# Optimization experiments

Measured on AMD Instinct MI355X. Metric: run time of the kernel, lower is better.

Reference implementation:

```python
import jax, jax.numpy as jnp
import numpy as np

# Module hyperparameters (init_kwargs)
RADIUS = 0.3
NSAMPLE = 64
NORMALIZE_XYZ = True

B, N, M, C = 8, 20000, 1024, 128  # batch, points, centers, feature channels


def setup_inputs() -> dict:
    key = jax.random.key(0)
    k1, k2, k3, k4, k5 = jax.random.split(key, 5)
    # points uniform in a side-2 cube -> each radius-0.3 ball holds ~280 pts
    xyz = jax.random.uniform(k1, (B, N, 3), jnp.float32) * 2.0
    new_xyz = jax.random.uniform(k2, (B, M, 3), jnp.float32) * 2.0
    batch_distances = jax.random.uniform(k3, (B, M), jnp.float32)
    inds = jax.random.randint(k4, (B, M), 0, N, jnp.int64)
    features = jax.random.normal(k5, (B, C, N), jnp.float32)
    return {"xyz": xyz, "new_xyz": new_xyz, "batch_distances": batch_distances,
            "inds": inds, "features": features}


def ball_query(xyz, new_xyz):
    """Standard pointnet2 ball query: first NSAMPLE indices with d^2 < r^2,
    remaining slots filled with the first in-range index. -> (B, M, NSAMPLE) int32."""
    n = xyz.shape[1]
    # (B, M, N) squared distances
    d2 = jnp.sum((new_xyz[:, :, None, :] - xyz[:, None, :, :]) ** 2, axis=-1)
    mask = d2 < (RADIUS * RADIUS)
    ar = jnp.arange(n, dtype=jnp.int32)
    # sort key: valid indices keep their index (in order), invalid pushed to back
    sort_key = jnp.where(mask, ar, ar + n)
    order = jnp.argsort(sort_key, axis=-1)[..., :NSAMPLE].astype(jnp.int32)
    cnt = jnp.sum(mask, axis=-1)  # (B, M) number of in-range points
    slot = jnp.arange(NSAMPLE, dtype=cnt.dtype)
    # slots beyond cnt are filled with the first valid index (0 if cnt == 0)
    idx = jnp.where(slot[None, None, :] < jnp.maximum(cnt, 1)[..., None],
                    order, order[..., :1])
    return idx


def reference(xyz, new_xyz, batch_distances, inds, features):
    # batch_distances / inds only accelerate the original cpp kernel; the math
    # is the plain radius search below.
    idx = ball_query(xyz, new_xyz)  # (B, M, S)
    # group xyz: (B, M, S, 3) -> (B, 3, M, S)
    grouped_xyz = jax.vmap(lambda pts, i: pts[i])(xyz, idx)
    grouped_xyz = jnp.transpose(grouped_xyz, (0, 3, 1, 2))
    grouped_xyz = grouped_xyz - jnp.transpose(new_xyz, (0, 2, 1))[..., None]
    if NORMALIZE_XYZ:
        grouped_xyz = grouped_xyz / RADIUS
    # group features: (B, C, M, S)
    grouped_features = jax.vmap(lambda f, i: f[:, i])(features, idx)
    new_features = jnp.concatenate([grouped_xyz, grouped_features], axis=1)
    return (new_features, idx)
```

## Files before the change

kernel.cpp:

```cpp
#include <hip/hip_runtime.h>

#define B_ 8
#define N_ 20000
#define M_ 1024
#define C_ 128
#define S_ 64
#define NCH_ 131
#define GD_ 7
#define NC_ (GD_*GD_*GD_)
#define SCALE_ 3.2f
#define NW_ 626
#define NWP_ 640

typedef float  vf4 __attribute__((ext_vector_type(4)));

__device__ __forceinline__ int cell_of(float x, float y, float z) {
    const int ix = (int)(x * SCALE_);
    const int iy = (int)(y * SCALE_);
    const int iz = (int)(z * SCALE_);
    return (ix * GD_ + iy) * GD_ + iz;
}

__global__ __launch_bounds__(1024) void build_grid(
    const float* __restrict__ xyz,
    float4* __restrict__ pts4,
    int* __restrict__ cst)
{
    const int b   = blockIdx.x;
    const int tid = threadIdx.x;
    __shared__ int hcnt[NC_];
    __shared__ int hstart[NC_ + 1];

    if (tid < NC_) hcnt[tid] = 0;
    __syncthreads();

    const float* xb = xyz + (size_t)b * N_ * 3;
    for (int i = tid; i < N_; i += 1024) {
        const float x = xb[3*i], y = xb[3*i+1], z = xb[3*i+2];
        atomicAdd(&hcnt[cell_of(x, y, z)], 1);
    }
    __syncthreads();

    if (tid == 0) {
        int run = 0;
        for (int c = 0; c < NC_; ++c) { hstart[c] = run; run += hcnt[c]; }
        hstart[NC_] = run;
    }
    __syncthreads();

    if (tid < NC_ + 1) cst[b * (NC_ + 1) + tid] = hstart[tid];
    if (tid < NC_) hcnt[tid] = hstart[tid];
    __syncthreads();

    for (int i = tid; i < N_; i += 1024) {
        const float x = xb[3*i], y = xb[3*i+1], z = xb[3*i+2];
        const int slot = atomicAdd(&hcnt[cell_of(x, y, z)], 1);
        float4 p; p.x = x; p.y = y; p.z = z; p.w = __int_as_float(i);
        pts4[(size_t)b * N_ + slot] = p;
    }
}

__global__ __launch_bounds__(512) void query_kernel(
    const float* __restrict__ xyz,
    const float* __restrict__ new_xyz,
    const float4* __restrict__ pts4,
    const int* __restrict__ cst,
    float* __restrict__ out,
    int* __restrict__ iws)
{
    const int tid  = threadIdx.x;
    const int w    = tid >> 6;
    const int lane = tid & 63;
    const int bm   = blockIdx.x * 8 + w;
    const int b    = bm >> 10;
    const int m    = bm & (M_ - 1);

    __shared__ unsigned bmap[8][NWP_];
    __shared__ int s_widx[8][S_];

    for (int k = lane; k < NWP_; k += 64) bmap[w][k] = 0u;

    const float cx = new_xyz[bm * 3 + 0];
    const float cy = new_xyz[bm * 3 + 1];
    const float cz = new_xyz[bm * 3 + 2];
    const float r2 = (float)(0.3 * 0.3);

    const int ix = (int)(cx * SCALE_);
    const int iy = (int)(cy * SCALE_);
    const int iz = (int)(cz * SCALE_);
    const int x0 = ix > 0 ? ix - 1 : 0, x1 = ix < GD_-1 ? ix + 1 : GD_-1;
    const int y0 = iy > 0 ? iy - 1 : 0, y1 = iy < GD_-1 ? iy + 1 : GD_-1;
    const int z0 = iz > 0 ? iz - 1 : 0, z1 = iz < GD_-1 ? iz + 1 : GD_-1;

    const float4* pb = pts4 + (size_t)b * N_;
    const int* cb = cst + b * (NC_ + 1);

    for (int xx = x0; xx <= x1; ++xx) {
        for (int yy = y0; yy <= y1; ++yy) {
            const int cid = (xx * GD_ + yy) * GD_;
            const int s = cb[cid + z0];
            const int e = cb[cid + z1 + 1];
            for (int i = s + lane; i < e; i += 64) {
                const float4 p = pb[i];
                const float dx = __fadd_rn(p.x, -cx);
                const float dy = __fadd_rn(p.y, -cy);
                const float dz = __fadd_rn(p.z, -cz);
                const float d2 = __fadd_rn(
                    __fadd_rn(__fmul_rn(dx, dx), __fmul_rn(dy, dy)),
                    __fmul_rn(dz, dz));
                if (d2 < r2) {
                    const int po = __float_as_int(p.w);
                    atomicOr(&bmap[w][po >> 5], 1u << (po & 31));
                }
            }
        }
    }

    int cnt = 0;
    for (int base = 0; base < NW_ && cnt < S_; base += 64) {
        const int wi = base + lane;
        const unsigned wv = (wi < NW_) ? bmap[w][wi] : 0u;
        const int c = __popc(wv);
        int p = c;
#pragma unroll
        for (int o = 1; o < 64; o <<= 1) {
            const int t = __shfl_up(p, o);
            if (lane >= o) p += t;
        }
        const int tot = __shfl(p, 63);
        int r = cnt + p - c;
        unsigned ww = wv;
        while (ww && r < S_) {
            const int bit = __ffs(ww) - 1;
            s_widx[w][r] = wi * 32 + bit;
            ++r;
            ww &= ww - 1;
        }
        cnt += tot;
    }

    {
        const int c = cnt < S_ ? cnt : S_;
        const int first = (c > 0) ? s_widx[w][0] : 0;
        if (lane >= c) s_widx[w][lane] = first;
    }

    const int n = s_widx[w][lane];
    const float* xb = xyz + (size_t)b * N_ * 3;

    float* out_idx = out + (size_t)B_ * NCH_ * M_ * S_;
    __builtin_nontemporal_store((float)n, &out_idx[(size_t)bm * S_ + lane]);
    iws[(size_t)bm * S_ + lane] = n;

    const float px = xb[n * 3 + 0];
    const float py = xb[n * 3 + 1];
    const float pz = xb[n * 3 + 2];
    __builtin_nontemporal_store((px - cx) / 0.3f,
        &out[(((size_t)b * NCH_ + 0) * M_ + m) * S_ + lane]);
    __builtin_nontemporal_store((py - cy) / 0.3f,
        &out[(((size_t)b * NCH_ + 1) * M_ + m) * S_ + lane]);
    __builtin_nontemporal_store((pz - cz) / 0.3f,
        &out[(((size_t)b * NCH_ + 2) * M_ + m) * S_ + lane]);
}

__global__ __launch_bounds__(256) void group_feat_kernel(
    const float* __restrict__ features,
    const int* __restrict__ iws,
    float* __restrict__ out)
{
    const int b  = blockIdx.x & 7;
    const int ch = blockIdx.x >> 3;

    __shared__ float slice[N_];

    const float* fb = features + ((size_t)b * C_ + ch) * N_;
    const vf4* fb4 = (const vf4*)fb;
    vf4* sl4 = (vf4*)slice;
    for (int i = threadIdx.x; i < N_ / 4; i += 256)
        sl4[i] = __builtin_nontemporal_load(&fb4[i]);
    __syncthreads();

    const int* ib = iws + (size_t)b * M_ * S_;
    float* ob = out + ((size_t)b * NCH_ + 3 + ch) * (size_t)(M_ * S_);
    for (int e = threadIdx.x * 4; e < M_ * S_; e += 256 * 4) {
        const int4 ii = *(const int4*)(ib + e);
        vf4 w;
        w.x = slice[ii.x]; w.y = slice[ii.y];
        w.z = slice[ii.z]; w.w = slice[ii.w];
        __builtin_nontemporal_store(w, (vf4*)(ob + e));
    }
}

__global__ __launch_bounds__(256) void qg_fused(
    const float* __restrict__ xyz,
    const float* __restrict__ new_xyz,
    const float* __restrict__ features,
    float* __restrict__ out)
{
    const int bm = blockIdx.x;
    const int b  = bm >> 10;
    const int m  = bm & (M_ - 1);
    const int tid = threadIdx.x;

    __shared__ int s_idx[S_];

    if (tid < 64) {
        const int lane = tid;
        const float cx = new_xyz[bm * 3 + 0];
        const float cy = new_xyz[bm * 3 + 1];
        const float cz = new_xyz[bm * 3 + 2];
        const float r2 = (float)(0.3 * 0.3);
        const float* xb = xyz + (size_t)b * N_ * 3;

        int cnt = 0;
        for (int base = 0; base < N_; base += 64) {
            const int n = base + lane;
            bool valid = false;
            if (n < N_) {
                const float dx = __fadd_rn(xb[n * 3 + 0], -cx);
                const float dy = __fadd_rn(xb[n * 3 + 1], -cy);
                const float dz = __fadd_rn(xb[n * 3 + 2], -cz);
                const float d2 = __fadd_rn(
                    __fadd_rn(__fmul_rn(dx, dx), __fmul_rn(dy, dy)),
                    __fmul_rn(dz, dz));
                valid = d2 < r2;
            }
            const unsigned long long mk = __ballot(valid);
            if (valid) {
                const int pos = cnt + __popcll(mk & ((1ull << lane) - 1ull));
                if (pos < S_) s_idx[pos] = n;
            }
            cnt += __popcll(mk);
            if (cnt >= S_) break;
        }
        const int c = cnt < S_ ? cnt : S_;
        const int first = (c > 0) ? s_idx[0] : 0;
        if (lane >= c) s_idx[lane] = first;

        float* out_idx = out + (size_t)B_ * NCH_ * M_ * S_;
        out_idx[(size_t)bm * S_ + lane] = (float)s_idx[lane];
    }
    __syncthreads();

    if (tid < 3 * S_) {
        const int ch = tid >> 6;
        const int s  = tid & 63;
        const int n  = s_idx[s];
        const float v = (xyz[((size_t)b * N_ + n) * 3 + ch] - new_xyz[bm * 3 + ch]) / 0.3f;
        out[(((size_t)b * NCH_ + ch) * M_ + m) * S_ + s] = v;
    }

    const int s  = tid & 63;
    const int cq = tid >> 6;
    const int n  = s_idx[s];
    const float* fb = features + (size_t)b * C_ * N_;
    float* ob = out + (((size_t)b * NCH_ + 3) * M_ + m) * S_ + s;
    for (int ch = cq; ch < C_; ch += 4) {
        ob[(size_t)ch * (M_ * S_)] = fb[(size_t)ch * N_ + n];
    }
}

extern "C" void kernel_launch(void* const* d_in, const int* in_sizes, int n_in,
                              void* d_out, int out_size, void* d_ws, size_t ws_size,
                              hipStream_t stream) {
    const float* xyz      = (const float*)d_in[0];
    const float* new_xyz  = (const float*)d_in[1];
    const float* features = (const float*)d_in[4];
    float* out = (float*)d_out;

    const size_t pts4_elems = (size_t)B_ * N_;
    const size_t cst_elems  = (size_t)B_ * (NC_ + 1);
    const size_t iws_elems  = (size_t)B_ * M_ * S_;
    const size_t need = pts4_elems * 16 + (cst_elems + iws_elems) * 4;

    if (ws_size < need) {
        qg_fused<<<B_ * M_, 256, 0, stream>>>(xyz, new_xyz, features, out);
        return;
    }
    float4* pts4 = (float4*)d_ws;
    int*    cst  = (int*)(pts4 + pts4_elems);
    int*    iws  = cst + cst_elems;

    build_grid<<<B_, 1024, 0, stream>>>(xyz, pts4, cst);
    query_kernel<<<(B_ * M_) / 8, 512, 0, stream>>>(xyz, new_xyz, pts4, cst, out, iws);
    group_feat_kernel<<<B_ * C_, 256, 0, stream>>>(features, iws, out);
}
```

Baseline: 136.7 us.

## Split grid build into parallel count, wave-scan, and global-atomic scatter kernels

The single per-batch grid build (8 blocks of 1024 threads, with a serial single-thread prefix sum) is replaced by three kernels. The first counts cells over 64 blocks of point slices, the second does a wave-parallel scan across slices per batch, and the third scatters points using global atomics. The aim is to spread the grid construction over more CUs and remove the serial scan. In exchange it adds two kernel launches and uses global rather than shared-memory atomics for the scatter, which also makes the order of points within a cell nondeterministic.

Result: faster. 133.6 us (-2.3%).

```diff
diff --git a/kernel.cpp b/kernel.cpp
--- a/kernel.cpp
+++ b/kernel.cpp
@@ -11,6 +11,8 @@
 #define SCALE_ 3.2f
 #define NW_ 626
 #define NWP_ 640
+#define SLICES_ 8
+#define SLPTS_ (N_ / SLICES_)
 
 typedef float  vf4 __attribute__((ext_vector_type(4)));
 
@@ -21,40 +23,65 @@
     return (ix * GD_ + iy) * GD_ + iz;
 }
 
-__global__ __launch_bounds__(1024) void build_grid(
+__global__ __launch_bounds__(256) void grid_count(
     const float* __restrict__ xyz,
-    float4* __restrict__ pts4,
-    int* __restrict__ cst)
-{
-    const int b   = blockIdx.x;
-    const int tid = threadIdx.x;
-    __shared__ int hcnt[NC_];
-    __shared__ int hstart[NC_ + 1];
-
-    if (tid < NC_) hcnt[tid] = 0;
+    int* __restrict__ part)
+{
+    const int blk = blockIdx.x;
+    const int b = blk >> 3, s = blk & 7;
+    __shared__ int h[NC_];
+    for (int i = threadIdx.x; i < NC_; i += 256) h[i] = 0;
     __syncthreads();
 
     const float* xb = xyz + (size_t)b * N_ * 3;
-    for (int i = tid; i < N_; i += 1024) {
+    const int p0 = s * SLPTS_, p1 = p0 + SLPTS_;
+    for (int i = p0 + threadIdx.x; i < p1; i += 256)
+        atomicAdd(&h[cell_of(xb[3*i], xb[3*i+1], xb[3*i+2])], 1);
+    __syncthreads();
+
+    int* pr = part + blk * NC_;
+    for (int i = threadIdx.x; i < NC_; i += 256) pr[i] = h[i];
+}
+
+__global__ __launch_bounds__(512) void grid_scan(
+    const int* __restrict__ part,
+    int* __restrict__ cst,
+    int* __restrict__ cur)
+{
+    const int w = threadIdx.x >> 6, lane = threadIdx.x & 63;
+    int run = 0;
+    for (int c0 = 0; c0 < NC_; c0 += 64) {
+        const int idx = c0 + lane;
+        int v = 0;
+        if (idx < NC_) {
+#pragma unroll
+            for (int s = 0; s < SLICES_; ++s) v += part[(w*SLICES_+s)*NC_ + idx];
+        }
+        int sc = v;
+#pragma unroll
+        for (int o = 1; o < 64; o <<= 1) {
+            const int t = __shfl_up(sc, o);
+            if (lane >= o) sc += t;
+        }
+        const int excl = run + sc - v;
+        if (idx < NC_) { cst[w*(NC_+1)+idx] = excl; cur[w*NC_+idx] = excl; }
+        run += __shfl(sc, 63);
+    }
+    if (lane == 0) cst[w*(NC_+1)+NC_] = run;
+}
+
+__global__ __launch_bounds__(256) void grid_scatter(
+    const float* __restrict__ xyz,
+    int* __restrict__ cur,
+    float4* __restrict__ pts4)
+{
+    const int blk = blockIdx.x;
+    const int b = blk >> 3, s = blk & 7;
+    const float* xb = xyz + (size_t)b * N_ * 3;
+    const int p0 = s * SLPTS_, p1 = p0 + SLPTS_;
+    for (int i = p0 + threadIdx.x; i < p1; i += 256) {
         const float x = xb[3*i], y = xb[3*i+1], z = xb[3*i+2];
-        atomicAdd(&hcnt[cell_of(x, y, z)], 1);
-    }
-    __syncthreads();
-
-    if (tid == 0) {
-        int run = 0;
-        for (int c = 0; c < NC_; ++c) { hstart[c] = run; run += hcnt[c]; }
-        hstart[NC_] = run;
-    }
-    __syncthreads();
-
-    if (tid < NC_ + 1) cst[b * (NC_ + 1) + tid] = hstart[tid];
-    if (tid < NC_) hcnt[tid] = hstart[tid];
-    __syncthreads();
-
-    for (int i = tid; i < N_; i += 1024) {
-        const float x = xb[3*i], y = xb[3*i+1], z = xb[3*i+2];
-        const int slot = atomicAdd(&hcnt[cell_of(x, y, z)], 1);
+        const int slot = atomicAdd(&cur[b*NC_ + cell_of(x, y, z)], 1);
         float4 p; p.x = x; p.y = y; p.z = z; p.w = __int_as_float(i);
         pts4[(size_t)b * N_ + slot] = p;
     }
@@ -270,8 +297,11 @@
 
     const size_t pts4_elems = (size_t)B_ * N_;
     const size_t cst_elems  = (size_t)B_ * (NC_ + 1);
+    const size_t cur_elems  = (size_t)B_ * NC_;
+    const size_t part_elems = (size_t)B_ * SLICES_ * NC_;
     const size_t iws_elems  = (size_t)B_ * M_ * S_;
-    const size_t need = pts4_elems * 16 + (cst_elems + iws_elems) * 4;
+    const size_t need = pts4_elems * 16 +
+                        (cst_elems + cur_elems + part_elems + iws_elems) * 4;
 
     if (ws_size < need) {
         qg_fused<<<B_ * M_, 256, 0, stream>>>(xyz, new_xyz, features, out);
@@ -279,9 +309,13 @@
     }
     float4* pts4 = (float4*)d_ws;
     int*    cst  = (int*)(pts4 + pts4_elems);
-    int*    iws  = cst + cst_elems;
-
-    build_grid<<<B_, 1024, 0, stream>>>(xyz, pts4, cst);
+    int*    cur  = cst + cst_elems;
+    int*    part = cur + cur_elems;
+    int*    iws  = part + part_elems;
+
+    grid_count  <<<B_ * SLICES_, 256, 0, stream>>>(xyz, part);
+    grid_scan   <<<1, 512, 0, stream>>>(part, cst, cur);
+    grid_scatter<<<B_ * SLICES_, 256, 0, stream>>>(xyz, cur, pts4);
     query_kernel<<<(B_ * M_) / 8, 512, 0, stream>>>(xyz, new_xyz, pts4, cst, out, iws);
     group_feat_kernel<<<B_ * C_, 256, 0, stream>>>(features, iws, out);
 }
```
